# Kernel tuning notes

Measured on AMD Instinct MI355X. Metric: run time of the kernel, lower is better.

Reference implementation:

```python
import jax, jax.numpy as jnp
import numpy as np

B, CIN, COUT, H, W = 8, 256, 256, 64, 64
K, STRIDE, PAD = 3, 1, 1


def setup_inputs() -> dict:
    key = jax.random.key(0)
    k1, k2, k3 = jax.random.split(key, 3)
    x = jax.random.normal(k1, (B, CIN, H, W), dtype=jnp.float32)
    offset = jax.random.normal(k2, (B, 2 * K * K, H, W), dtype=jnp.float32)
    weight = jax.random.normal(k3, (COUT, CIN, K, K), dtype=jnp.float32) * 0.05
    return {"x": x, "offset": offset, "weight": weight}


def _deform_conv2d(x, offset, weight):
    # x: [B, C, H, W]; offset: [B, 2*K*K, Ho, Wo] (y,x interleaved per tap, mmcv layout)
    Bn, C, Hh, Ww = x.shape
    Ho, Wo = Hh, Ww  # stride=1, pad=1, k=3
    K2 = K * K
    ki, kj = jnp.meshgrid(jnp.arange(K), jnp.arange(K), indexing="ij")
    ki = ki.reshape(-1).astype(jnp.float32)  # [K2] row offset of tap
    kj = kj.reshape(-1).astype(jnp.float32)
    hh = jnp.arange(Ho, dtype=jnp.float32)
    ww = jnp.arange(Wo, dtype=jnp.float32)
    # base sampling grid per tap: [K2, Ho, Wo]
    base_y = ki[:, None, None] + hh[None, :, None] * STRIDE - PAD
    base_x = kj[:, None, None] + ww[None, None, :] * STRIDE - PAD
    off = offset.reshape(Bn, K2, 2, Ho, Wo)
    py = base_y[None] + off[:, :, 0]  # [B, K2, Ho, Wo]
    px = base_x[None] + off[:, :, 1]

    y0 = jnp.floor(py)
    x0 = jnp.floor(px)

    def gather(im, yy, xx):
        # im: [C, H, W]; yy, xx: [K2, Ho, Wo] -> [C, K2, Ho, Wo]
        return im[:, yy, xx]

    vgather = jax.vmap(gather)  # over batch

    val = jnp.zeros((Bn, C, K2, Ho, Wo), dtype=x.dtype)
    for dy in (0.0, 1.0):
        for dx in (0.0, 1.0):
            yi = y0 + dy
            xi = x0 + dx
            wgt = (1.0 - jnp.abs(py - yi)) * (1.0 - jnp.abs(px - xi))
            valid = (yi >= 0) & (yi < Hh) & (xi >= 0) & (xi < Ww)
            yc = jnp.clip(yi, 0, Hh - 1).astype(jnp.int32)
            xc = jnp.clip(xi, 0, Ww - 1).astype(jnp.int32)
            v = vgather(x, yc, xc)  # [B, C, K2, Ho, Wo]
            val = val + v * (wgt * valid)[:, None]

    w2 = weight.reshape(weight.shape[0], C, K2)
    return jnp.einsum("bckhw,ock->bohw", val, w2)


def reference(x, offset, weight):
    return jax.nn.relu(_deform_conv2d(x, offset, weight))
```

## Files before the change

### kernel.cpp

```cpp
#include <hip/hip_runtime.h>


#define B_   8
#define C_   256
#define H_   64
#define W_   64
#define K2_  9
#define HW_  4096
#define NC4  64

typedef __fp16 f16x2 __attribute__((ext_vector_type(2)));
typedef __fp16 f16x8 __attribute__((ext_vector_type(8)));
typedef float  f32x4 __attribute__((ext_vector_type(4)));

static __device__ __forceinline__ f16x2 u2h(unsigned u) {
    union { unsigned u; f16x2 h; } v; v.u = u; return v.h;
}
static __device__ __forceinline__ unsigned h2u(f16x2 h) {
    union { unsigned u; f16x2 h; } v; v.h = h; return v.u;
}

__global__ __launch_bounds__(256) void wpack_kernel(
    const float* __restrict__ w, unsigned short* __restrict__ wA) {
    const int t = blockIdx.x * 256 + threadIdx.x;
    if (t >= C_ * C_ * K2_) return;
    const int k = t % 9;
    const int c = (t / 9) & 255;
    const int o = t / (9 * 256);
    const int cc = c >> 5, lg = (c >> 3) & 3, e = c & 7;
    const int t16 = o >> 4, lr = o & 15;
    const int dst = e + 8 * (lr + 16 * (lg + 4 * (t16 + 16 * (cc + 8 * k))));
    const __fp16 h = (__fp16)w[t];
    unsigned short us;
    __builtin_memcpy(&us, &h, 2);
    wA[dst] = us;
}

__global__ __launch_bounds__(256) void xptpack_kernel(
    const float* __restrict__ x, uint4* __restrict__ xpt) {
    const int bid = blockIdx.x;
    const int b = bid >> 6, y = bid & 63;
    const int tid = threadIdx.x;
    __shared__ unsigned pr[64][256];

    const float* xb = x + ((size_t)(b * C_ + tid) * H_ + y) * W_;
#pragma unroll
    for (int i = 0; i < 16; ++i) {
        const int c0 = i * 4;
        const float4 v = *(const float4*)(xb + c0);
        const float nxt = xb[(c0 == 60) ? 63 : c0 + 4];
        pr[c0 + 0][tid] = h2u(__builtin_amdgcn_cvt_pkrtz(v.x, v.y));
        pr[c0 + 1][tid] = h2u(__builtin_amdgcn_cvt_pkrtz(v.y, v.z));
        pr[c0 + 2][tid] = h2u(__builtin_amdgcn_cvt_pkrtz(v.z, v.w));
        pr[c0 + 3][tid] = h2u(__builtin_amdgcn_cvt_pkrtz(v.w, nxt));
    }
    __syncthreads();
    const int lane = tid & 63, wv = tid >> 6;
    uint4* dst = xpt + ((size_t)b * HW_ + (size_t)y * 64) * NC4;
#pragma unroll
    for (int i = 0; i < 16; ++i) {
        const int col = wv * 16 + i;
        const uint4 cell = *(const uint4*)&pr[col][lane * 4];
        dst[(size_t)col * NC4 + lane] = cell;
    }
}

template<int MODE>
__global__ __launch_bounds__(512, 4) void deform_main(
    const float* __restrict__ x, const uint4* __restrict__ xpt,
    const float* __restrict__ offset, const unsigned short* __restrict__ wA,
    float* __restrict__ out)
{
    const int bid = blockIdx.x;
    const int b = bid & 7, ho = bid >> 3;
    const int tid = threadIdx.x;
    const int lane = tid & 63;
    const int wv   = tid >> 6;
    const int lr = lane & 15, lg = (lane >> 4) & 3;

    __shared__ unsigned short gaddr[K2_][W_];
    __shared__ uint2 gw2[K2_][W_];
    __shared__ alignas(16) unsigned short btile[2][W_][256];

    for (int e = tid; e < K2_ * W_; e += 512) {
        const int k = e >> 6, wo = e & 63;
        const float offy = offset[((b * 18 + 2 * k    ) * H_ + ho) * W_ + wo];
        const float offx = offset[((b * 18 + 2 * k + 1) * H_ + ho) * W_ + wo];
        const float py = (float)(k / 3 + ho - 1) + offy;
        const float px = (float)(k % 3 + wo - 1) + offx;
        const float y0f = floorf(py), x0f = floorf(px);
        const int   y0 = (int)y0f,   x0 = (int)x0f;
        const float fy = py - y0f,   fx = px - x0f;
        const float wy0 = (y0 >= 0  && y0 < H_)     ? 1.f - fy : 0.f;
        const float wy1 = (y0 >= -1 && y0 < H_ - 1) ? fy       : 0.f;
        const float wx0 = (x0 >= 0  && x0 < W_)     ? 1.f - fx : 0.f;
        const float wx1 = (x0 >= -1 && x0 < W_ - 1) ? fx       : 0.f;
        const int ys = min(max(y0, 0), H_ - 2);
        const int xs = min(max(x0, 0), W_ - 2);
        const float qy0 = (ys == y0 ? wy0 : 0.f) + (ys == y0 + 1 ? wy1 : 0.f);
        const float qy1 = (ys + 1 == y0 ? wy0 : 0.f) + (ys + 1 == y0 + 1 ? wy1 : 0.f);
        const float qx0 = (xs == x0 ? wx0 : 0.f) + (xs == x0 + 1 ? wx1 : 0.f);
        const float qx1 = (xs + 1 == x0 ? wx0 : 0.f) + (xs + 1 == x0 + 1 ? wx1 : 0.f);
        gaddr[k][wo] = (unsigned short)(ys * W_ + xs);
        gw2[k][wo] = make_uint2(
            h2u(__builtin_amdgcn_cvt_pkrtz(qy0 * qx0, qy0 * qx1)),
            h2u(__builtin_amdgcn_cvt_pkrtz(qy1 * qx0, qy1 * qx1)));
    }
    __syncthreads();

    f32x4 acc[2][4];
#pragma unroll
    for (int m = 0; m < 2; ++m)
#pragma unroll
        for (int n = 0; n < 4; ++n) acc[m][n] = (f32x4)0.f;

    const __fp16* wAh = (const __fp16*)wA;
    const uint4* xptb = xpt + (size_t)b * HW_ * NC4;

#define A_LOAD(k_, cc_, AS, AT) {                                              \
    const __fp16* ap_ = wAh +                                                  \
        (((size_t)((k_) * 8 + (cc_)) * 16 + wv * 2) * 64 + lane) * 8;          \
    AS = *(const f16x8*)ap_;                                                   \
    AT = *(const f16x8*)(ap_ + 512); }

#define G_ISSUE(k_, j_, QT, QB) {                                              \
    const int qp_ = gaddr[k_][wv * 8 + (j_)];                                  \
    QT = xptb[(size_t)qp_ * NC4 + lane];                                       \
    QB = xptb[(size_t)(qp_ + 64) * NC4 + lane]; }

#define G_CONSUME(k_, j_, QT, QB, SB) {                                        \
    const int p_ = wv * 8 + (j_);                                              \
    const uint2 wp_ = gw2[k_][p_];                                             \
    const f16x2 wt_ = u2h(wp_.x), wb_ = u2h(wp_.y);                            \
    const float v0_ = __builtin_amdgcn_fdot2(u2h(QT.x), wt_,                   \
        __builtin_amdgcn_fdot2(u2h(QB.x), wb_, 0.f, false), false);            \
    const float v1_ = __builtin_amdgcn_fdot2(u2h(QT.y), wt_,                   \
        __builtin_amdgcn_fdot2(u2h(QB.y), wb_, 0.f, false), false);            \
    const float v2_ = __builtin_amdgcn_fdot2(u2h(QT.z), wt_,                   \
        __builtin_amdgcn_fdot2(u2h(QB.z), wb_, 0.f, false), false);            \
    const float v3_ = __builtin_amdgcn_fdot2(u2h(QT.w), wt_,                   \
        __builtin_amdgcn_fdot2(u2h(QB.w), wb_, 0.f, false), false);            \
    const unsigned pk0_ = h2u(__builtin_amdgcn_cvt_pkrtz(v0_, v1_));           \
    const unsigned pk1_ = h2u(__builtin_amdgcn_cvt_pkrtz(v2_, v3_));           \
    const int phys_ = (lane >> 1) ^ (p_ & 7);                                  \
    *(uint2*)((char*)&btile[SB][p_][0] + phys_ * 16 + (lane & 1) * 8) =        \
        make_uint2(pk0_, pk1_); }

#define MFMA_CC(cc_, MB, AS, AT) {                                             \
    _Pragma("unroll")                                                          \
    for (int nt = 0; nt < 4; ++nt) {                                           \
        const int pix_ = nt * 16 + lr;                                         \
        const int phys_ = ((cc_) * 4 + lg) ^ (pix_ & 7);                       \
        const f16x8 bv_ = *(const f16x8*)                                      \
            ((const char*)&btile[MB][pix_][0] + phys_ * 16);                   \
        acc[0][nt] = __builtin_amdgcn_mfma_f32_16x16x32_f16(                   \
            AS, bv_, acc[0][nt], 0, 0, 0);                                     \
        acc[1][nt] = __builtin_amdgcn_mfma_f32_16x16x32_f16(                   \
            AT, bv_, acc[1][nt], 0, 0, 0);                                     \
    } }

#define STAGE(k_, SB)                                                          \
    G_CONSUME(k_, 0, qT0, qB0, SB) G_ISSUE(k_, 4, qT0, qB0)                    \
    G_CONSUME(k_, 1, qT1, qB1, SB) G_ISSUE(k_, 5, qT1, qB1)                    \
    G_CONSUME(k_, 2, qT2, qB2, SB) G_ISSUE(k_, 6, qT2, qB2)                    \
    G_CONSUME(k_, 3, qT3, qB3, SB) G_ISSUE(k_, 7, qT3, qB3)                    \
    G_CONSUME(k_, 4, qT0, qB0, SB) G_CONSUME(k_, 5, qT1, qB1, SB)              \
    G_CONSUME(k_, 6, qT2, qB2, SB) G_CONSUME(k_, 7, qT3, qB3, SB)

    if constexpr (MODE == 0) {
        uint4 qT0, qB0, qT1, qB1, qT2, qB2, qT3, qB3;
        f16x8 aS0, aT0, aS1, aT1, aS2, aT2, aS3, aT3;

        A_LOAD(0, 0, aS0, aT0)
        A_LOAD(0, 1, aS1, aT1)
        G_ISSUE(0, 0, qT0, qB0) G_ISSUE(0, 1, qT1, qB1)
        G_ISSUE(0, 2, qT2, qB2) G_ISSUE(0, 3, qT3, qB3)
        STAGE(0, 0)
        asm volatile("s_waitcnt lgkmcnt(0)" ::: "memory");
        __builtin_amdgcn_s_barrier();

        for (int k = 0; k < K2_; ++k) {
            const int mb = k & 1;
            A_LOAD(k, 2, aS2, aT2) MFMA_CC(0, mb, aS0, aT0)
            A_LOAD(k, 3, aS3, aT3) MFMA_CC(1, mb, aS1, aT1)
            A_LOAD(k, 4, aS0, aT0) MFMA_CC(2, mb, aS2, aT2)
            A_LOAD(k, 5, aS1, aT1) MFMA_CC(3, mb, aS3, aT3)
            A_LOAD(k, 6, aS2, aT2) MFMA_CC(4, mb, aS0, aT0)
            A_LOAD(k, 7, aS3, aT3) MFMA_CC(5, mb, aS1, aT1)
            if (k < K2_ - 1) {
                A_LOAD(k + 1, 0, aS0, aT0)
                A_LOAD(k + 1, 1, aS1, aT1)
                G_ISSUE(k + 1, 0, qT0, qB0) G_ISSUE(k + 1, 1, qT1, qB1)
                G_ISSUE(k + 1, 2, qT2, qB2) G_ISSUE(k + 1, 3, qT3, qB3)
            }
            MFMA_CC(6, mb, aS2, aT2)
            MFMA_CC(7, mb, aS3, aT3)
            if (k < K2_ - 1) {
                const int sb = (k + 1) & 1;
                STAGE(k + 1, sb)
            }
            asm volatile("s_waitcnt lgkmcnt(0)" ::: "memory");
            __builtin_amdgcn_s_barrier();
        }
    } else {
        for (int k = 0; k < K2_; ++k) {
            const int bb = k & 1;
#pragma unroll
            for (int j = 0; j < 8; ++j) {
                const int p_ = wv * 8 + j;
                const int qp = gaddr[k][p_];
                const uint2 wp_ = gw2[k][p_];
                const f16x2 wt_ = u2h(wp_.x), wb_ = u2h(wp_.y);
                const float w00 = (float)wt_.x, w01 = (float)wt_.y;
                const float w10 = (float)wb_.x, w11 = (float)wb_.y;
                float vv[4];
#pragma unroll
                for (int e2 = 0; e2 < 4; ++e2) {
                    const float* pl = x + ((size_t)(b * C_ + lane * 4 + e2)) * HW_;
                    vv[e2] = w00 * pl[qp] + w01 * pl[qp + 1]
                           + w10 * pl[qp + 64] + w11 * pl[qp + 65];
                }
                const unsigned pk0 = h2u(__builtin_amdgcn_cvt_pkrtz(vv[0], vv[1]));
                const unsigned pk1 = h2u(__builtin_amdgcn_cvt_pkrtz(vv[2], vv[3]));
                const int phys_ = (lane >> 1) ^ (p_ & 7);
                *(uint2*)((char*)&btile[bb][p_][0] + phys_ * 16 + (lane & 1) * 8) =
                    make_uint2(pk0, pk1);
            }
            __syncthreads();
#pragma unroll
            for (int cc = 0; cc < 8; ++cc) {
                f16x8 a0, a1;
                A_LOAD(k, cc, a0, a1)
                MFMA_CC(cc, bb, a0, a1)
            }
            __syncthreads();
        }
    }

    const size_t ob = (size_t)b * C_ * HW_ + (size_t)ho * W_;
#pragma unroll
    for (int mt = 0; mt < 2; ++mt) {
        const int o0 = wv * 32 + mt * 16 + lg * 4;
#pragma unroll
        for (int nt = 0; nt < 4; ++nt) {
            const int wo = nt * 16 + lr;
#pragma unroll
            for (int r = 0; r < 4; ++r)
                out[ob + (size_t)(o0 + r) * HW_ + wo] =
                    fmaxf(acc[mt][nt][r], 0.f);
        }
    }
#undef A_LOAD
#undef G_ISSUE
#undef G_CONSUME
#undef MFMA_CC
#undef STAGE
}

extern "C" void kernel_launch(void* const* d_in, const int* in_sizes, int n_in,
                              void* d_out, int out_size, void* d_ws, size_t ws_size,
                              hipStream_t stream) {
    const float* x      = (const float*)d_in[0];
    const float* offset = (const float*)d_in[1];
    const float* weight = (const float*)d_in[2];
    float* out          = (float*)d_out;

    const size_t wA_bytes = (size_t)K2_ * C_ * C_ * 2;
    const size_t xp_off   = wA_bytes;
    const size_t xp_bytes = (size_t)B_ * HW_ * NC4 * 16;
    const size_t need     = xp_off + xp_bytes;

    unsigned short* wAp = (unsigned short*)d_ws;
    uint4*          xpp = (uint4*)((char*)d_ws + xp_off);

    wpack_kernel<<<(C_ * C_ * K2_ + 255) / 256, 256, 0, stream>>>(weight, wAp);

    if (ws_size >= need) {
        xptpack_kernel<<<B_ * H_, 256, 0, stream>>>(x, xpp);
        deform_main<0><<<512, 512, 0, stream>>>(x, xpp, offset, wAp, out);
    } else {
        deform_main<1><<<512, 512, 0, stream>>>(x, xpp, offset, wAp, out);
    }
}
```

Measured before the change: 87.83 us.

## Process two output rows per block, interleave gathers with MFMAs, merge pack kernels

Each block of the main kernel now computes two output rows (128 pixels) instead of one. Every weight fragment loaded from global memory therefore feeds twice as many MFMAs, and the grid shrinks to 256 blocks. Because the tile needs more than 140 KB of shared memory, it moves to dynamic LDS. The bilinear gather and staging for the next tap are now spread between the MFMA groups of the current tap to hide global latency. The weight-pack and x-pack kernels are merged into one launch. The trade-off is more accumulator registers, one block per CU, and no spare blocks to hide tail latency.

```diff
diff --git a/kernel.cpp b/kernel.cpp
--- a/kernel.cpp
+++ b/kernel.cpp
@@ -20,29 +20,30 @@
     union { unsigned u; f16x2 h; } v; v.h = h; return v.u;
 }
 
-__global__ __launch_bounds__(256) void wpack_kernel(
-    const float* __restrict__ w, unsigned short* __restrict__ wA) {
-    const int t = blockIdx.x * 256 + threadIdx.x;
-    if (t >= C_ * C_ * K2_) return;
-    const int k = t % 9;
-    const int c = (t / 9) & 255;
-    const int o = t / (9 * 256);
-    const int cc = c >> 5, lg = (c >> 3) & 3, e = c & 7;
-    const int t16 = o >> 4, lr = o & 15;
-    const int dst = e + 8 * (lr + 16 * (lg + 4 * (t16 + 16 * (cc + 8 * k))));
-    const __fp16 h = (__fp16)w[t];
-    unsigned short us;
-    __builtin_memcpy(&us, &h, 2);
-    wA[dst] = us;
-}
-
-__global__ __launch_bounds__(256) void xptpack_kernel(
-    const float* __restrict__ x, uint4* __restrict__ xpt) {
+__global__ __launch_bounds__(256) void pack_kernel(
+    const float* __restrict__ x, const float* __restrict__ w,
+    uint4* __restrict__ xpt, unsigned short* __restrict__ wA)
+{
+    const int tid = threadIdx.x;
+    if (blockIdx.x >= 512) {
+        const int t = (blockIdx.x - 512) * 256 + tid;
+        if (t < C_ * C_ * K2_) {
+            const int k = t % 9;
+            const int c = (t / 9) & 255;
+            const int o = t / (9 * 256);
+            const int cc = c >> 5, lg = (c >> 3) & 3, e = c & 7;
+            const int t16 = o >> 4, lr = o & 15;
+            const int dst = e + 8 * (lr + 16 * (lg + 4 * (t16 + 16 * (cc + 8 * k))));
+            const __fp16 h = (__fp16)w[t];
+            unsigned short us;
+            __builtin_memcpy(&us, &h, 2);
+            wA[dst] = us;
+        }
+        return;
+    }
     const int bid = blockIdx.x;
     const int b = bid >> 6, y = bid & 63;
-    const int tid = threadIdx.x;
     __shared__ unsigned pr[64][256];
-
     const float* xb = x + ((size_t)(b * C_ + tid) * H_ + y) * W_;
 #pragma unroll
     for (int i = 0; i < 16; ++i) {
@@ -60,30 +61,33 @@
 #pragma unroll
     for (int i = 0; i < 16; ++i) {
         const int col = wv * 16 + i;
-        const uint4 cell = *(const uint4*)&pr[col][lane * 4];
-        dst[(size_t)col * NC4 + lane] = cell;
+        dst[(size_t)col * NC4 + lane] = *(const uint4*)&pr[col][lane * 4];
     }
 }
 
 template<int MODE>
-__global__ __launch_bounds__(512, 4) void deform_main(
+__global__ __launch_bounds__(512, 2) void deform_main(
     const float* __restrict__ x, const uint4* __restrict__ xpt,
     const float* __restrict__ offset, const unsigned short* __restrict__ wA,
     float* __restrict__ out)
 {
+    extern __shared__ char smem[];
+    unsigned short (*btile)[128][256] =
+        (unsigned short (*)[128][256])smem;
+    uint2*          gw2   = (uint2*)(smem + 131072);
+    unsigned short* gaddr = (unsigned short*)(smem + 140288);
+
     const int bid = blockIdx.x;
-    const int b = bid & 7, ho = bid >> 3;
+    const int b = bid & 7, ho2 = bid >> 3;
     const int tid = threadIdx.x;
     const int lane = tid & 63;
     const int wv   = tid >> 6;
     const int lr = lane & 15, lg = (lane >> 4) & 3;
 
-    __shared__ unsigned short gaddr[K2_][W_];
-    __shared__ uint2 gw2[K2_][W_];
-    __shared__ alignas(16) unsigned short btile[2][W_][256];
-
-    for (int e = tid; e < K2_ * W_; e += 512) {
-        const int k = e >> 6, wo = e & 63;
+    for (int e = tid; e < K2_ * 128; e += 512) {
+        const int k = e >> 7, p = e & 127;
+        const int row = p >> 6, wo = p & 63;
+        const int ho = ho2 * 2 + row;
         const float offy = offset[((b * 18 + 2 * k    ) * H_ + ho) * W_ + wo];
         const float offx = offset[((b * 18 + 2 * k + 1) * H_ + ho) * W_ + wo];
         const float py = (float)(k / 3 + ho - 1) + offy;
@@ -101,18 +105,18 @@
         const float qy1 = (ys + 1 == y0 ? wy0 : 0.f) + (ys + 1 == y0 + 1 ? wy1 : 0.f);
         const float qx0 = (xs == x0 ? wx0 : 0.f) + (xs == x0 + 1 ? wx1 : 0.f);
         const float qx1 = (xs + 1 == x0 ? wx0 : 0.f) + (xs + 1 == x0 + 1 ? wx1 : 0.f);
-        gaddr[k][wo] = (unsigned short)(ys * W_ + xs);
-        gw2[k][wo] = make_uint2(
+        gaddr[k * 128 + p] = (unsigned short)(ys * W_ + xs);
+        gw2[k * 128 + p] = make_uint2(
             h2u(__builtin_amdgcn_cvt_pkrtz(qy0 * qx0, qy0 * qx1)),
             h2u(__builtin_amdgcn_cvt_pkrtz(qy1 * qx0, qy1 * qx1)));
     }
     __syncthreads();
 
-    f32x4 acc[2][4];
+    f32x4 acc[2][8];
 #pragma unroll
     for (int m = 0; m < 2; ++m)
 #pragma unroll
-        for (int n = 0; n < 4; ++n) acc[m][n] = (f32x4)0.f;
+        for (int n = 0; n < 8; ++n) acc[m][n] = (f32x4)0.f;
 
     const __fp16* wAh = (const __fp16*)wA;
     const uint4* xptb = xpt + (size_t)b * HW_ * NC4;
@@ -123,14 +127,14 @@
     AS = *(const f16x8*)ap_;                                                   \
     AT = *(const f16x8*)(ap_ + 512); }
 
-#define G_ISSUE(k_, j_, QT, QB) {                                              \
-    const int qp_ = gaddr[k_][wv * 8 + (j_)];                                  \
+#define G_ISSUE(t_, j_, QT, QB) {                                              \
+    const int qp_ = gaddr[(t_) * 128 + wv * 16 + (j_)];                        \
     QT = xptb[(size_t)qp_ * NC4 + lane];                                       \
     QB = xptb[(size_t)(qp_ + 64) * NC4 + lane]; }
 
-#define G_CONSUME(k_, j_, QT, QB, SB) {                                        \
-    const int p_ = wv * 8 + (j_);                                              \
-    const uint2 wp_ = gw2[k_][p_];                                             \
+#define G_CONSUME(t_, j_, QT, QB, SB) {                                        \
+    const int p_ = wv * 16 + (j_);                                             \
+    const uint2 wp_ = gw2[(t_) * 128 + p_];                                    \
     const f16x2 wt_ = u2h(wp_.x), wb_ = u2h(wp_.y);                            \
     const float v0_ = __builtin_amdgcn_fdot2(u2h(QT.x), wt_,                   \
         __builtin_amdgcn_fdot2(u2h(QB.x), wb_, 0.f, false), false);            \
@@ -148,7 +152,7 @@
 
 #define MFMA_CC(cc_, MB, AS, AT) {                                             \
     _Pragma("unroll")                                                          \
-    for (int nt = 0; nt < 4; ++nt) {                                           \
+    for (int nt = 0; nt < 8; ++nt) {                                           \
         const int pix_ = nt * 16 + lr;                                         \
         const int phys_ = ((cc_) * 4 + lg) ^ (pix_ & 7);                       \
         const f16x8 bv_ = *(const f16x8*)                                      \
@@ -159,14 +163,6 @@
             AT, bv_, acc[1][nt], 0, 0, 0);                                     \
     } }
 
-#define STAGE(k_, SB)                                                          \
-    G_CONSUME(k_, 0, qT0, qB0, SB) G_ISSUE(k_, 4, qT0, qB0)                    \
-    G_CONSUME(k_, 1, qT1, qB1, SB) G_ISSUE(k_, 5, qT1, qB1)                    \
-    G_CONSUME(k_, 2, qT2, qB2, SB) G_ISSUE(k_, 6, qT2, qB2)                    \
-    G_CONSUME(k_, 3, qT3, qB3, SB) G_ISSUE(k_, 7, qT3, qB3)                    \
-    G_CONSUME(k_, 4, qT0, qB0, SB) G_CONSUME(k_, 5, qT1, qB1, SB)              \
-    G_CONSUME(k_, 6, qT2, qB2, SB) G_CONSUME(k_, 7, qT3, qB3, SB)
-
     if constexpr (MODE == 0) {
         uint4 qT0, qB0, qT1, qB1, qT2, qB2, qT3, qB3;
         f16x8 aS0, aT0, aS1, aT1, aS2, aT2, aS3, aT3;
@@ -175,41 +171,78 @@
         A_LOAD(0, 1, aS1, aT1)
         G_ISSUE(0, 0, qT0, qB0) G_ISSUE(0, 1, qT1, qB1)
         G_ISSUE(0, 2, qT2, qB2) G_ISSUE(0, 3, qT3, qB3)
-        STAGE(0, 0)
+        G_CONSUME(0, 0, qT0, qB0, 0)  G_ISSUE(0, 4, qT0, qB0)
+        G_CONSUME(0, 1, qT1, qB1, 0)  G_ISSUE(0, 5, qT1, qB1)
+        G_CONSUME(0, 2, qT2, qB2, 0)  G_ISSUE(0, 6, qT2, qB2)
+        G_CONSUME(0, 3, qT3, qB3, 0)  G_ISSUE(0, 7, qT3, qB3)
+        G_CONSUME(0, 4, qT0, qB0, 0)  G_ISSUE(0, 8, qT0, qB0)
+        G_CONSUME(0, 5, qT1, qB1, 0)  G_ISSUE(0, 9, qT1, qB1)
+        G_CONSUME(0, 6, qT2, qB2, 0)  G_ISSUE(0, 10, qT2, qB2)
+        G_CONSUME(0, 7, qT3, qB3, 0)  G_ISSUE(0, 11, qT3, qB3)
+        G_CONSUME(0, 8, qT0, qB0, 0)  G_ISSUE(0, 12, qT0, qB0)
+        G_CONSUME(0, 9, qT1, qB1, 0)  G_ISSUE(0, 13, qT1, qB1)
+        G_CONSUME(0, 10, qT2, qB2, 0) G_ISSUE(0, 14, qT2, qB2)
+        G_CONSUME(0, 11, qT3, qB3, 0) G_ISSUE(0, 15, qT3, qB3)
+        G_CONSUME(0, 12, qT0, qB0, 0) G_CONSUME(0, 13, qT1, qB1, 0)
+        G_CONSUME(0, 14, qT2, qB2, 0) G_CONSUME(0, 15, qT3, qB3, 0)
+        G_ISSUE(1, 0, qT0, qB0) G_ISSUE(1, 1, qT1, qB1)
+        G_ISSUE(1, 2, qT2, qB2) G_ISSUE(1, 3, qT3, qB3)
         asm volatile("s_waitcnt lgkmcnt(0)" ::: "memory");
         __builtin_amdgcn_s_barrier();
 
         for (int k = 0; k < K2_; ++k) {
-            const int mb = k & 1;
-            A_LOAD(k, 2, aS2, aT2) MFMA_CC(0, mb, aS0, aT0)
-            A_LOAD(k, 3, aS3, aT3) MFMA_CC(1, mb, aS1, aT1)
-            A_LOAD(k, 4, aS0, aT0) MFMA_CC(2, mb, aS2, aT2)
-            A_LOAD(k, 5, aS1, aT1) MFMA_CC(3, mb, aS3, aT3)
-            A_LOAD(k, 6, aS2, aT2) MFMA_CC(4, mb, aS0, aT0)
-            A_LOAD(k, 7, aS3, aT3) MFMA_CC(5, mb, aS1, aT1)
-            if (k < K2_ - 1) {
-                A_LOAD(k + 1, 0, aS0, aT0)
-                A_LOAD(k + 1, 1, aS1, aT1)
-                G_ISSUE(k + 1, 0, qT0, qB0) G_ISSUE(k + 1, 1, qT1, qB1)
-                G_ISSUE(k + 1, 2, qT2, qB2) G_ISSUE(k + 1, 3, qT3, qB3)
+            const int mb = k & 1, sb = mb ^ 1;
+            const int st = (k < K2_ - 1);
+            const int kn = st ? (k + 1) : k;
+
+            A_LOAD(k, 2, aS2, aT2)
+            if (st) { G_CONSUME(kn, 0, qT0, qB0, sb) G_ISSUE(kn, 4, qT0, qB0) }
+            MFMA_CC(0, mb, aS0, aT0)
+            A_LOAD(k, 3, aS3, aT3)
+            if (st) { G_CONSUME(kn, 1, qT1, qB1, sb) G_ISSUE(kn, 5, qT1, qB1) }
+            MFMA_CC(1, mb, aS1, aT1)
+            A_LOAD(k, 4, aS0, aT0)
+            if (st) { G_CONSUME(kn, 2, qT2, qB2, sb) G_ISSUE(kn, 6, qT2, qB2) }
+            MFMA_CC(2, mb, aS2, aT2)
+            A_LOAD(k, 5, aS1, aT1)
+            if (st) { G_CONSUME(kn, 3, qT3, qB3, sb) G_ISSUE(kn, 7, qT3, qB3) }
+            MFMA_CC(3, mb, aS3, aT3)
+            A_LOAD(k, 6, aS2, aT2)
+            if (st) { G_CONSUME(kn, 4, qT0, qB0, sb) G_ISSUE(kn, 8, qT0, qB0) }
+            MFMA_CC(4, mb, aS0, aT0)
+            A_LOAD(k, 7, aS3, aT3)
+            if (st) { G_CONSUME(kn, 5, qT1, qB1, sb) G_ISSUE(kn, 9, qT1, qB1) }
+            MFMA_CC(5, mb, aS1, aT1)
+            if (st) {
+                A_LOAD(kn, 0, aS0, aT0)
+                A_LOAD(kn, 1, aS1, aT1)
+                G_CONSUME(kn, 6, qT2, qB2, sb) G_ISSUE(kn, 10, qT2, qB2)
             }
             MFMA_CC(6, mb, aS2, aT2)
+            if (st) { G_CONSUME(kn, 7, qT3, qB3, sb) G_ISSUE(kn, 11, qT3, qB3) }
             MFMA_CC(7, mb, aS3, aT3)
-            if (k < K2_ - 1) {
-                const int sb = (k + 1) & 1;
-                STAGE(k + 1, sb)
+            if (st) {
+                G_CONSUME(kn, 8, qT0, qB0, sb)  G_ISSUE(kn, 12, qT0, qB0)
+                G_CONSUME(kn, 9, qT1, qB1, sb)  G_ISSUE(kn, 13, qT1, qB1)
+                G_CONSUME(kn, 10, qT2, qB2, sb) G_ISSUE(kn, 14, qT2, qB2)
+                G_CONSUME(kn, 11, qT3, qB3, sb) G_ISSUE(kn, 15, qT3, qB3)
+                G_CONSUME(kn, 12, qT0, qB0, sb) G_CONSUME(kn, 13, qT1, qB1, sb)
+                G_CONSUME(kn, 14, qT2, qB2, sb) G_CONSUME(kn, 15, qT3, qB3, sb)
+                if (k < K2_ - 2) {
+                    G_ISSUE(k + 2, 0, qT0, qB0) G_ISSUE(k + 2, 1, qT1, qB1)
+                    G_ISSUE(k + 2, 2, qT2, qB2) G_ISSUE(k + 2, 3, qT3, qB3)
+                }
             }
             asm volatile("s_waitcnt lgkmcnt(0)" ::: "memory");
             __builtin_amdgcn_s_barrier();
         }
     } else {
         for (int k = 0; k < K2_; ++k) {
-            const int bb = k & 1;
-#pragma unroll
-            for (int j = 0; j < 8; ++j) {
-                const int p_ = wv * 8 + j;
-                const int qp = gaddr[k][p_];
-                const uint2 wp_ = gw2[k][p_];
+#pragma unroll
+            for (int j = 0; j < 16; ++j) {
+                const int p_ = wv * 16 + j;
+                const int qp = gaddr[k * 128 + p_];
+                const uint2 wp_ = gw2[k * 128 + p_];
                 const f16x2 wt_ = u2h(wp_.x), wb_ = u2h(wp_.y);
                 const float w00 = (float)wt_.x, w01 = (float)wt_.y;
                 const float w10 = (float)wb_.x, w11 = (float)wb_.y;
@@ -223,7 +256,7 @@
                 const unsigned pk0 = h2u(__builtin_amdgcn_cvt_pkrtz(vv[0], vv[1]));
                 const unsigned pk1 = h2u(__builtin_amdgcn_cvt_pkrtz(vv[2], vv[3]));
                 const int phys_ = (lane >> 1) ^ (p_ & 7);
-                *(uint2*)((char*)&btile[bb][p_][0] + phys_ * 16 + (lane & 1) * 8) =
+                *(uint2*)((char*)&btile[0][p_][0] + phys_ * 16 + (lane & 1) * 8) =
                     make_uint2(pk0, pk1);
             }
             __syncthreads();
@@ -231,22 +264,24 @@
             for (int cc = 0; cc < 8; ++cc) {
                 f16x8 a0, a1;
                 A_LOAD(k, cc, a0, a1)
-                MFMA_CC(cc, bb, a0, a1)
+                MFMA_CC(cc, 0, a0, a1)
             }
             __syncthreads();
         }
     }
 
-    const size_t ob = (size_t)b * C_ * HW_ + (size_t)ho * W_;
+    const size_t ob = (size_t)b * C_ * HW_;
+    const int hbase = ho2 * 2;
 #pragma unroll
     for (int mt = 0; mt < 2; ++mt) {
         const int o0 = wv * 32 + mt * 16 + lg * 4;
 #pragma unroll
-        for (int nt = 0; nt < 4; ++nt) {
-            const int wo = nt * 16 + lr;
+        for (int nt = 0; nt < 8; ++nt) {
+            const int pix = nt * 16 + lr;
+            const int row = pix >> 6, wo = pix & 63;
 #pragma unroll
             for (int r = 0; r < 4; ++r)
-                out[ob + (size_t)(o0 + r) * HW_ + wo] =
+                out[ob + (size_t)(o0 + r) * HW_ + (size_t)(hbase + row) * W_ + wo] =
                     fmaxf(acc[mt][nt][r], 0.f);
         }
     }
@@ -254,7 +289,6 @@
 #undef G_ISSUE
 #undef G_CONSUME
 #undef MFMA_CC
-#undef STAGE
 }
 
 extern "C" void kernel_launch(void* const* d_in, const int* in_sizes, int n_in,
@@ -273,12 +307,12 @@
     unsigned short* wAp = (unsigned short*)d_ws;
     uint4*          xpp = (uint4*)((char*)d_ws + xp_off);
 
-    wpack_kernel<<<(C_ * C_ * K2_ + 255) / 256, 256, 0, stream>>>(weight, wAp);
-
+    pack_kernel<<<512 + 2304, 256, 0, stream>>>(x, weight, xpp, wAp);
+
+    const size_t lds = 131072 + 9216 + 2304;
     if (ws_size >= need) {
-        xptpack_kernel<<<B_ * H_, 256, 0, stream>>>(x, xpp);
-        deform_main<0><<<512, 512, 0, stream>>>(x, xpp, offset, wAp, out);
+        deform_main<0><<<256, 512, lds, stream>>>(x, xpp, offset, wAp, out);
     } else {
-        deform_main<1><<<512, 512, 0, stream>>>(x, xpp, offset, wAp, out);
-    }
-}
+        deform_main<1><<<256, 512, lds, stream>>>(x, xpp, offset, wAp, out);
+    }
+}
```

Result: faster. 74.25 us (-15.5%).
